# Performance work log

Hardware: AMD Instinct MI355X
Metric: run time of the kernel (lower is better)

## Reference

```python
import jax, jax.numpy as jnp
import numpy as np
import math

B, N, CS, CZ, CH, H, PQK, PV = 1, 1024, 384, 128, 16, 12, 4, 8
INF, EPS = 1e5, 1e-8


def quat_to_rot(q):
    w, x, y, z = q[..., 0], q[..., 1], q[..., 2], q[..., 3]
    r = jnp.stack([
        1 - 2 * (y * y + z * z), 2 * (x * y - w * z), 2 * (x * z + w * y),
        2 * (x * y + w * z), 1 - 2 * (x * x + z * z), 2 * (y * z - w * x),
        2 * (x * z - w * y), 2 * (y * z + w * x), 1 - 2 * (x * x + y * y),
    ], axis=-1)
    return r.reshape(q.shape[:-1] + (3, 3))


def setup_inputs() -> dict:
    key = jax.random.key(0)
    ks = jax.random.split(key, 12)
    sc = 0.02
    s = jax.random.normal(ks[0], (B, N, CS), jnp.float32)
    z = jax.random.normal(ks[1], (B, N, N, CZ), jnp.float32)
    quat = jax.random.normal(ks[2], (B, N, 4), jnp.float32)
    rot = quat_to_rot(quat / jnp.linalg.norm(quat, axis=-1, keepdims=True))
    trans = jax.random.normal(ks[3], (B, N, 3), jnp.float32)
    mask = jnp.ones((B, N), jnp.float32)
    wq = jax.random.normal(ks[4], (CS, H * CH), jnp.float32) * sc
    bq = jnp.zeros((H * CH,), jnp.float32)
    wkv = jax.random.normal(ks[5], (CS, 2 * H * CH), jnp.float32) * sc
    bkv = jnp.zeros((2 * H * CH,), jnp.float32)
    wqp = jax.random.normal(ks[6], (CS, H * PQK * 3), jnp.float32) * sc
    bqp = jnp.zeros((H * PQK * 3,), jnp.float32)
    wkvp = jax.random.normal(ks[7], (CS, H * (PQK + PV) * 3), jnp.float32) * sc
    bkvp = jnp.zeros((H * (PQK + PV) * 3,), jnp.float32)
    wb = jax.random.normal(ks[8], (CZ, H), jnp.float32) * sc
    bb = jnp.zeros((H,), jnp.float32)
    head_w = jax.random.normal(ks[9], (H,), jnp.float32) * 0.1 + 0.5413  # softplus^-1(1)
    dcat = H * (CZ + CH + PV * 4)
    wout = jax.random.normal(ks[10], (dcat, CS), jnp.float32) * sc
    bout = jnp.zeros((CS,), jnp.float32)
    return dict(s=s, z=z, rot=rot, trans=trans, mask=mask, wq=wq, bq=bq,
                wkv=wkv, bkv=bkv, wqp=wqp, bqp=bqp, wkvp=wkvp, bkvp=bkvp,
                wb=wb, bb=bb, head_w=head_w, wout=wout, bout=bout)


def reference(s, z, rot, trans, mask, wq, bq, wkv, bkv, wqp, bqp, wkvp, bkvp,
              wb, bb, head_w, wout, bout):
    # scalar q/k/v: [B,N,H,CH]
    q = (s @ wq + bq).reshape(B, N, H, CH)
    kv = (s @ wkv + bkv).reshape(B, N, H, 2 * CH)
    k, v = kv[..., :CH], kv[..., CH:]

    def make_pts(raw, P):
        # raw layout: [x-coords | y-coords | z-coords], each of width H*P
        pts = jnp.swapaxes(raw.reshape(B, N, 3, H * P), -1, -2)  # [B,N,H*P,3]
        pts = jnp.einsum('bnxy,bnpy->bnpx', rot, pts) + trans[:, :, None, :]
        return pts.reshape(B, N, H, P, 3)

    q_pts = make_pts(s @ wqp + bqp, PQK)                 # [B,N,H,PQK,3] global frame
    kv_pts = make_pts(s @ wkvp + bkvp, PQK + PV)
    k_pts, v_pts = kv_pts[..., :PQK, :], kv_pts[..., PQK:, :]

    # scalar attention + pair bias: [B,H,N,N]
    a = jnp.einsum('bihc,bjhc->bhij', q, k) * math.sqrt(1.0 / (3 * CH))
    bias = z @ wb + bb                                    # [B,N,N,H]
    a = a + math.sqrt(1.0 / 3) * jnp.transpose(bias, (0, 3, 1, 2))

    # point attention via ||q-k||^2 = |q|^2 + |k|^2 - 2 q.k (summed over pts & xyz)
    hw = jax.nn.softplus(head_w) * math.sqrt(1.0 / (3 * (PQK * 9.0 / 2)))  # [H]
    qn = jnp.sum(q_pts ** 2, axis=(-1, -2))               # [B,N,H]
    kn = jnp.sum(k_pts ** 2, axis=(-1, -2))
    cross = jnp.einsum('bihpx,bjhpx->bhij', q_pts, k_pts)
    sqd = (jnp.transpose(qn, (0, 2, 1))[..., None]
           + jnp.transpose(kn, (0, 2, 1))[:, :, None, :]
           - 2.0 * cross)                                 # [B,H,N,N]
    a = a - 0.5 * hw[None, :, None, None] * sqd

    sqm = INF * (mask[:, :, None] * mask[:, None, :] - 1.0)  # [B,N,N]
    a = jax.nn.softmax(a + sqm[:, None], axis=-1)

    # outputs
    o = jnp.einsum('bhij,bjhc->bihc', a, v).reshape(B, N, H * CH)
    o_pt = jnp.einsum('bhij,bjhpx->bihpx', a, v_pts)      # [B,N,H,PV,3] global
    o_pt = jnp.einsum('bnyx,bnhpy->bnhpx', rot, o_pt - trans[:, :, None, None, :])  # invert_apply
    o_pt_norm = jnp.sqrt(jnp.sum(o_pt ** 2, axis=-1) + EPS).reshape(B, N, H * PV)
    o_pt3 = o_pt.reshape(B, N, H * PV, 3)
    o_pair = jnp.einsum('bhij,bijc->bihc', a, z).reshape(B, N, H * CZ)

    cat = jnp.concatenate(
        [o, o_pt3[..., 0], o_pt3[..., 1], o_pt3[..., 2], o_pt_norm, o_pair], axis=-1)
    return cat @ wout + bout
```

## Files before the change

### kernel.cpp

```cpp
#include <hip/hip_runtime.h>
#include <hip/hip_bf16.h>
#include <math.h>

#define NN   1024
#define CS   384
#define CZ   128
#define HH   12
#define HCH  192
#define QPR  144
#define DCAT 2112
#define PROJW 1152
#define INF_ 100000.0f

#define SC_QK 0.14433756729740643f
#define SC_B  0.5773502691896258f
#define SC_PT 0.13608276348795434f

__device__ __forceinline__ float dot4(float4 a, float4 b) {
  return a.x * b.x + a.y * b.y + a.z * b.z + a.w * b.w;
}
__device__ __forceinline__ float bf2f(unsigned short u) {
  unsigned int v = ((unsigned int)u) << 16;
  float f; __builtin_memcpy(&f, &v, 4); return f;
}
__device__ __forceinline__ unsigned short f2bf(float f) {
  __hip_bfloat16 h = __float2bfloat16(f);
  unsigned short u; __builtin_memcpy(&u, &h, 2); return u;
}

__global__ void prep(const float* __restrict__ wb, const float* __restrict__ head_w,
                     float* __restrict__ wb_t, float* __restrict__ hw)
{
  int t = threadIdx.x;
  for (int idx = t; idx < CZ * HH; idx += 256) {
    int c = idx % HH == idx % HH ? idx / HH : 0;
    int h = idx - c * HH;
    wb_t[h * CZ + c] = wb[idx];
  }
  if (t < HH) {
    float x = head_w[t];
    float sp = (x > 20.f) ? x : log1pf(__expf(x));
    hw[t] = sp * SC_PT;
  }
}

__global__ __launch_bounds__(256) void proj_all(
    const float* __restrict__ s,
    const float* __restrict__ wq, const float* __restrict__ bq,
    const float* __restrict__ wkv, const float* __restrict__ bkv,
    const float* __restrict__ wqp, const float* __restrict__ bqp,
    const float* __restrict__ wkvp, const float* __restrict__ bkvp,
    float* __restrict__ proj)
{
  __shared__ float s_lds[8 * CS];
  const int n0 = blockIdx.x * 8;
  for (int idx = threadIdx.x; idx < 8 * CS; idx += 256)
    s_lds[idx] = s[(size_t)(n0 + idx / CS) * CS + (idx % CS)];
  __syncthreads();

  const int gc = blockIdx.y * 128 + (threadIdx.x & 31) * 4;
  const int rg = threadIdx.x >> 5;
  const float* wp; const float* bp; int OUT, lc;
  if (gc < 192)      { wp = wq;   bp = bq;   OUT = 192; lc = gc; }
  else if (gc < 576) { wp = wkv;  bp = bkv;  OUT = 384; lc = gc - 192; }
  else if (gc < 720) { wp = wqp;  bp = bqp;  OUT = 144; lc = gc - 576; }
  else               { wp = wkvp; bp = bkvp; OUT = 432; lc = gc - 720; }

  float a0 = 0.f, a1 = 0.f, a2 = 0.f, a3 = 0.f;
  const float* srow = &s_lds[rg * CS];
#pragma unroll 4
  for (int kk = 0; kk < CS; kk++) {
    float sv = srow[kk];
    float4 w4 = *reinterpret_cast<const float4*>(&wp[(size_t)kk * OUT + lc]);
    a0 += sv * w4.x; a1 += sv * w4.y; a2 += sv * w4.z; a3 += sv * w4.w;
  }
  float* o = proj + (size_t)(n0 + rg) * PROJW + gc;
  o[0] = a0 + bp[lc]; o[1] = a1 + bp[lc + 1];
  o[2] = a2 + bp[lc + 2]; o[3] = a3 + bp[lc + 3];
}

__global__ __launch_bounds__(256) void ipa_transform(
    const float* __restrict__ proj, const float* __restrict__ rot,
    const float* __restrict__ trans,
    float* __restrict__ kc, float* __restrict__ vc,
    float* __restrict__ q_pts, float* __restrict__ kpc,
    float* __restrict__ vpc, float* __restrict__ qn, float* __restrict__ knc)
{
  const int n = blockIdx.x, tid = threadIdx.x;
  const float* pr = proj + (size_t)n * PROJW;
  __shared__ float R[9], T[3], sq_q[48], sq_k[48];
  if (tid < 9) R[tid] = rot[n * 9 + tid];
  if (tid < 3) T[tid] = trans[n * 3 + tid];
  __syncthreads();
  if (tid < HCH) {
    int h = tid >> 4, c = tid & 15;
    kc[(size_t)(h * 16 + c) * NN + n] = pr[192 + h * 32 + c];
    vc[(size_t)(h * 16 + c) * NN + n] = pr[192 + h * 32 + 16 + c];
  }
  if (tid < 48) {
    float r0 = pr[576 + tid], r1 = pr[576 + 48 + tid], r2 = pr[576 + 96 + tid];
    float x = R[0] * r0 + R[1] * r1 + R[2] * r2 + T[0];
    float y = R[3] * r0 + R[4] * r1 + R[5] * r2 + T[1];
    float z = R[6] * r0 + R[7] * r1 + R[8] * r2 + T[2];
    q_pts[(size_t)n * QPR + tid * 3 + 0] = x;
    q_pts[(size_t)n * QPR + tid * 3 + 1] = y;
    q_pts[(size_t)n * QPR + tid * 3 + 2] = z;
    sq_q[tid] = x * x + y * y + z * z;
  }
  if (tid >= 64 && tid < 208) {
    int t = tid - 64;
    float r0 = pr[720 + t], r1 = pr[720 + 144 + t], r2 = pr[720 + 288 + t];
    float x = R[0] * r0 + R[1] * r1 + R[2] * r2 + T[0];
    float y = R[3] * r0 + R[4] * r1 + R[5] * r2 + T[1];
    float z = R[6] * r0 + R[7] * r1 + R[8] * r2 + T[2];
    int h = t / 12, pp = t % 12;
    if (pp < 4) {
      int d = pp * 3;
      kpc[(size_t)(h * 12 + d + 0) * NN + n] = x;
      kpc[(size_t)(h * 12 + d + 1) * NN + n] = y;
      kpc[(size_t)(h * 12 + d + 2) * NN + n] = z;
      sq_k[h * 4 + pp] = x * x + y * y + z * z;
    } else {
      int d = (pp - 4) * 3;
      vpc[(size_t)(h * 24 + d + 0) * NN + n] = x;
      vpc[(size_t)(h * 24 + d + 1) * NN + n] = y;
      vpc[(size_t)(h * 24 + d + 2) * NN + n] = z;
    }
  }
  __syncthreads();
  if (tid < HH) {
    float a = 0.f, b = 0.f;
#pragma unroll
    for (int p = 0; p < 4; p++) { a += sq_q[tid * 4 + p]; b += sq_k[tid * 4 + p]; }
    qn[n * HH + tid] = a;
    knc[(size_t)tid * NN + n] = b;
  }
}

__global__ __launch_bounds__(256) void bias_pass(
    const float* __restrict__ z, const float* __restrict__ wb_t,
    __hip_bfloat16* __restrict__ B)
{
  __shared__ float wb_s[HH * CZ];
  __shared__ float bias_s[HH * 128];
  const int i = blockIdx.y;
  const int jb = blockIdx.x * 128;
  const int tid = threadIdx.x;
  const int jl = tid >> 2, csub = tid & 3;

  for (int e = tid; e < HH * CZ; e += 256) wb_s[e] = wb_t[e];
  __syncthreads();

  const float* zb = z + ((size_t)i * NN + jb + jl) * CZ + csub * 4;
  float4 zq0[8], zq1[8];
#pragma unroll
  for (int k8 = 0; k8 < 8; k8++)
    zq0[k8] = *reinterpret_cast<const float4*>(&zb[k8 * 16]);
#pragma unroll
  for (int k8 = 0; k8 < 8; k8++)
    zq1[k8] = *reinterpret_cast<const float4*>(&zb[(size_t)64 * CZ + k8 * 16]);

  float bd0[HH], bd1[HH];
#pragma unroll
  for (int h = 0; h < HH; h++) { bd0[h] = 0.f; bd1[h] = 0.f; }

#pragma unroll
  for (int k8 = 0; k8 < 8; k8++) {
    const int c = csub * 4 + k8 * 16;
#pragma unroll
    for (int h = 0; h < HH; h++) {
      float4 wv = *reinterpret_cast<const float4*>(&wb_s[h * CZ + c]);
      bd0[h] += dot4(zq0[k8], wv);
      bd1[h] += dot4(zq1[k8], wv);
    }
  }
#pragma unroll
  for (int h = 0; h < HH; h++) {
    bd0[h] += __shfl_xor(bd0[h], 1); bd0[h] += __shfl_xor(bd0[h], 2);
    bd1[h] += __shfl_xor(bd1[h], 1); bd1[h] += __shfl_xor(bd1[h], 2);
  }
  if (csub == 0) {
#pragma unroll
    for (int h = 0; h < HH; h++) {
      bias_s[h * 128 + jl] = bd0[h];
      bias_s[h * 128 + 64 + jl] = bd1[h];
    }
  }
  __syncthreads();
  for (int e = tid; e < HH * 128; e += 256) {
    int h = e >> 7, j2 = e & 127;
    B[((size_t)i * HH + h) * NN + jb + j2] = __float2bfloat16(bias_s[e]);
  }
}

__global__ __launch_bounds__(256) void ipa_attn(
    const float* __restrict__ kc, const float* __restrict__ kpc,
    const float* __restrict__ knc, const float* __restrict__ vc,
    const float* __restrict__ vpc, const float* __restrict__ proj,
    const float* __restrict__ q_pts, const float* __restrict__ qn,
    const float* __restrict__ bb, const float* __restrict__ hw,
    const float* __restrict__ mask,
    __hip_bfloat16* __restrict__ A, float* __restrict__ cat,
    float* __restrict__ optb)
{
  const int h = blockIdx.y;
  const int i = blockIdx.x * 4 + (threadIdx.x >> 6);
  const int lane = threadIdx.x & 63;

  const float* qb = proj + (size_t)i * PROJW + h * 16;
  const float4 q0 = *reinterpret_cast<const float4*>(qb);
  const float4 q1 = *reinterpret_cast<const float4*>(qb + 4);
  const float4 q2 = *reinterpret_cast<const float4*>(qb + 8);
  const float4 q3 = *reinterpret_cast<const float4*>(qb + 12);
  const float* pb = q_pts + (size_t)i * QPR + h * 12;
  const float4 p0 = *reinterpret_cast<const float4*>(pb);
  const float4 p1 = *reinterpret_cast<const float4*>(pb + 4);
  const float4 p2 = *reinterpret_cast<const float4*>(pb + 8);
  const float qnv = qn[i * HH + h];
  const float bbv = bb[h];
  const float hwv = hw[h];
  const float mi = mask[i];

  const float* kch  = kc  + (size_t)h * 16 * NN;
  const float* kpch = kpc + (size_t)h * 12 * NN;
  const float* knch = knc + (size_t)h * NN;
  const float* vch  = vc  + (size_t)h * 16 * NN;
  const float* vpch = vpc + (size_t)h * 24 * NN;
  __hip_bfloat16* Arow = A + ((size_t)i * HH + h) * NN;

  float4 av[4];
#pragma unroll
  for (int t = 0; t < 4; t++) {
    const int j = t * 256 + lane * 4;
    float4 d = {0, 0, 0, 0};
#pragma unroll
    for (int c = 0; c < 16; c++) {
      const float qc = (c < 4 ? (&q0.x)[c] : c < 8 ? (&q1.x)[c - 4]
                       : c < 12 ? (&q2.x)[c - 8] : (&q3.x)[c - 12]);
      float4 kv = *reinterpret_cast<const float4*>(&kch[(size_t)c * NN + j]);
      d.x += qc * kv.x; d.y += qc * kv.y; d.z += qc * kv.z; d.w += qc * kv.w;
    }
    float4 cr = {0, 0, 0, 0};
#pragma unroll
    for (int dd = 0; dd < 12; dd++) {
      const float pc = (dd < 4 ? (&p0.x)[dd] : dd < 8 ? (&p1.x)[dd - 4]
                        : (&p2.x)[dd - 8]);
      float4 kv = *reinterpret_cast<const float4*>(&kpch[(size_t)dd * NN + j]);
      cr.x += pc * kv.x; cr.y += pc * kv.y; cr.z += pc * kv.z; cr.w += pc * kv.w;
    }
    float4 kn4 = *reinterpret_cast<const float4*>(&knch[j]);
    ushort4 bu = *reinterpret_cast<const ushort4*>(&Arow[j]);
    float4 m4 = *reinterpret_cast<const float4*>(&mask[j]);
    av[t].x = SC_QK * d.x + SC_B * (bf2f(bu.x) + bbv)
              - 0.5f * hwv * (qnv + kn4.x - 2.f * cr.x) + INF_ * (mi * m4.x - 1.f);
    av[t].y = SC_QK * d.y + SC_B * (bf2f(bu.y) + bbv)
              - 0.5f * hwv * (qnv + kn4.y - 2.f * cr.y) + INF_ * (mi * m4.y - 1.f);
    av[t].z = SC_QK * d.z + SC_B * (bf2f(bu.z) + bbv)
              - 0.5f * hwv * (qnv + kn4.z - 2.f * cr.z) + INF_ * (mi * m4.z - 1.f);
    av[t].w = SC_QK * d.w + SC_B * (bf2f(bu.w) + bbv)
              - 0.5f * hwv * (qnv + kn4.w - 2.f * cr.w) + INF_ * (mi * m4.w - 1.f);
  }

  float m = av[0].x;
#pragma unroll
  for (int t = 0; t < 4; t++) {
    m = fmaxf(m, av[t].x); m = fmaxf(m, av[t].y);
    m = fmaxf(m, av[t].z); m = fmaxf(m, av[t].w);
  }
  for (int off = 32; off; off >>= 1) m = fmaxf(m, __shfl_xor(m, off));
  float ssum = 0.f;
#pragma unroll
  for (int t = 0; t < 4; t++) {
    av[t].x = __expf(av[t].x - m); ssum += av[t].x;
    av[t].y = __expf(av[t].y - m); ssum += av[t].y;
    av[t].z = __expf(av[t].z - m); ssum += av[t].z;
    av[t].w = __expf(av[t].w - m); ssum += av[t].w;
  }
  for (int off = 32; off; off >>= 1) ssum += __shfl_xor(ssum, off);
  const float inv = 1.f / ssum;
#pragma unroll
  for (int t = 0; t < 4; t++) {
    const int j = t * 256 + lane * 4;
    av[t].x *= inv; av[t].y *= inv; av[t].z *= inv; av[t].w *= inv;
    ushort4 st;
    st.x = f2bf(av[t].x); st.y = f2bf(av[t].y);
    st.z = f2bf(av[t].z); st.w = f2bf(av[t].w);
    *reinterpret_cast<ushort4*>(&Arow[j]) = st;
  }

  float oacc[16], wacc[24];
#pragma unroll
  for (int c = 0; c < 16; c++) oacc[c] = 0.f;
#pragma unroll
  for (int d = 0; d < 24; d++) wacc[d] = 0.f;
#pragma unroll
  for (int t = 0; t < 4; t++) {
    const int j = t * 256 + lane * 4;
    const float4 a4 = av[t];
#pragma unroll
    for (int c = 0; c < 16; c++) {
      float4 vv = *reinterpret_cast<const float4*>(&vch[(size_t)c * NN + j]);
      oacc[c] += dot4(a4, vv);
    }
#pragma unroll
    for (int d = 0; d < 24; d++) {
      float4 wv = *reinterpret_cast<const float4*>(&vpch[(size_t)d * NN + j]);
      wacc[d] += dot4(a4, wv);
    }
  }
  for (int off = 32; off; off >>= 1) {
#pragma unroll
    for (int c = 0; c < 16; c++) oacc[c] += __shfl_xor(oacc[c], off);
#pragma unroll
    for (int d = 0; d < 24; d++) wacc[d] += __shfl_xor(wacc[d], off);
  }
  if (lane == 0) {
    float* cr = cat + (size_t)i * DCAT + h * 16;
#pragma unroll
    for (int c = 0; c < 16; c++) cr[c] = oacc[c];
    float* ob = optb + ((size_t)i * HH + h) * 24;
#pragma unroll
    for (int d = 0; d < 24; d++) ob[d] = wacc[d];
  }
}

__global__ __launch_bounds__(256) void opair_pass(
    const float* __restrict__ z, const __hip_bfloat16* __restrict__ A,
    float* __restrict__ partial)
{
  __shared__ float A_ls[256 * HH];
  __shared__ float red[HH * CZ];
  const int sp = blockIdx.x, i = blockIdx.y;
  const int jb = sp * 256;
  const int tid = threadIdx.x;
  const int c4 = (tid & 31) * 4, jsub = tid >> 5;

  for (int e = tid; e < HH * 64; e += 256) {
    int h = e >> 6, j4 = (e & 63) * 4;
    ushort4 au = *reinterpret_cast<const ushort4*>(
        &A[((size_t)i * HH + h) * NN + jb + j4]);
    A_ls[(j4 + 0) * HH + h] = bf2f(au.x);
    A_ls[(j4 + 1) * HH + h] = bf2f(au.y);
    A_ls[(j4 + 2) * HH + h] = bf2f(au.z);
    A_ls[(j4 + 3) * HH + h] = bf2f(au.w);
  }
  for (int e = tid; e < HH * CZ; e += 256) red[e] = 0.f;
  __syncthreads();

  float4 acc[HH];
#pragma unroll
  for (int h = 0; h < HH; h++) acc[h] = make_float4(0.f, 0.f, 0.f, 0.f);

  const float* zrow = z + ((size_t)i * NN + jb + jsub * 32) * CZ + c4;
  const float* arow = &A_ls[jsub * 32 * HH];
  for (int j0 = 0; j0 < 32; j0 += 4) {
#pragma unroll
    for (int jj = 0; jj < 4; jj++) {
      const int j = j0 + jj;
      float4 zq = *reinterpret_cast<const float4*>(&zrow[(size_t)j * CZ]);
      float4 a0 = *reinterpret_cast<const float4*>(&arow[j * HH]);
      float4 a1 = *reinterpret_cast<const float4*>(&arow[j * HH + 4]);
      float4 a2 = *reinterpret_cast<const float4*>(&arow[j * HH + 8]);
      acc[0].x += a0.x * zq.x; acc[0].y += a0.x * zq.y;
      acc[0].z += a0.x * zq.z; acc[0].w += a0.x * zq.w;
      acc[1].x += a0.y * zq.x; acc[1].y += a0.y * zq.y;
      acc[1].z += a0.y * zq.z; acc[1].w += a0.y * zq.w;
      acc[2].x += a0.z * zq.x; acc[2].y += a0.z * zq.y;
      acc[2].z += a0.z * zq.z; acc[2].w += a0.z * zq.w;
      acc[3].x += a0.w * zq.x; acc[3].y += a0.w * zq.y;
      acc[3].z += a0.w * zq.z; acc[3].w += a0.w * zq.w;
      acc[4].x += a1.x * zq.x; acc[4].y += a1.x * zq.y;
      acc[4].z += a1.x * zq.z; acc[4].w += a1.x * zq.w;
      acc[5].x += a1.y * zq.x; acc[5].y += a1.y * zq.y;
      acc[5].z += a1.y * zq.z; acc[5].w += a1.y * zq.w;
      acc[6].x += a1.z * zq.x; acc[6].y += a1.z * zq.y;
      acc[6].z += a1.z * zq.z; acc[6].w += a1.z * zq.w;
      acc[7].x += a1.w * zq.x; acc[7].y += a1.w * zq.y;
      acc[7].z += a1.w * zq.z; acc[7].w += a1.w * zq.w;
      acc[8].x += a2.x * zq.x; acc[8].y += a2.x * zq.y;
      acc[8].z += a2.x * zq.z; acc[8].w += a2.x * zq.w;
      acc[9].x += a2.y * zq.x; acc[9].y += a2.y * zq.y;
      acc[9].z += a2.y * zq.z; acc[9].w += a2.y * zq.w;
      acc[10].x += a2.z * zq.x; acc[10].y += a2.z * zq.y;
      acc[10].z += a2.z * zq.z; acc[10].w += a2.z * zq.w;
      acc[11].x += a2.w * zq.x; acc[11].y += a2.w * zq.y;
      acc[11].z += a2.w * zq.z; acc[11].w += a2.w * zq.w;
    }
  }
  for (int s = 0; s < 8; s++) {
    __syncthreads();
    if (jsub == s) {
#pragma unroll
      for (int h = 0; h < HH; h++) {
        red[h * CZ + c4 + 0] += acc[h].x;
        red[h * CZ + c4 + 1] += acc[h].y;
        red[h * CZ + c4 + 2] += acc[h].z;
        red[h * CZ + c4 + 3] += acc[h].w;
      }
    }
  }
  __syncthreads();
  float* pp = partial + ((size_t)(i * 4 + sp)) * (HH * CZ);
  for (int e = tid; e < HH * CZ; e += 256) pp[e] = red[e];
}

__global__ __launch_bounds__(256) void opair_reduce(
    const float* __restrict__ partial, const float* __restrict__ optb,
    const float* __restrict__ rot, const float* __restrict__ trans,
    float* __restrict__ cat)
{
  const int i = blockIdx.x, tid = threadIdx.x;
  __shared__ float R_s[9], T_s[3];
  if (tid < 9) R_s[tid] = rot[i * 9 + tid];
  if (tid < 3) T_s[tid] = trans[i * 3 + tid];
  __syncthreads();

  const float* pp = partial + ((size_t)i * 4) * (HH * CZ);
  for (int e = tid; e < HH * CZ; e += 256) {
    float v = pp[e] + pp[HH * CZ + e] + pp[2 * HH * CZ + e] + pp[3 * HH * CZ + e];
    cat[(size_t)i * DCAT + 576 + e] = v;
  }
  if (tid < 96) {
    int h = tid >> 3, p = tid & 7;
    const float* ob = optb + ((size_t)i * HH + h) * 24 + p * 3;
    float gx = ob[0] - T_s[0];
    float gy = ob[1] - T_s[1];
    float gz = ob[2] - T_s[2];
    float lx = R_s[0] * gx + R_s[3] * gy + R_s[6] * gz;
    float ly = R_s[1] * gx + R_s[4] * gy + R_s[7] * gz;
    float lz = R_s[2] * gx + R_s[5] * gy + R_s[8] * gz;
    float* catr = cat + (size_t)i * DCAT;
    catr[192 + 0 * 96 + h * 8 + p] = lx;
    catr[192 + 1 * 96 + h * 8 + p] = ly;
    catr[192 + 2 * 96 + h * 8 + p] = lz;
    catr[480 + h * 8 + p] = sqrtf(lx * lx + ly * ly + lz * lz + 1e-8f);
  }
}

__global__ __launch_bounds__(256) void out_gemm(
    const float* __restrict__ cat, const float* __restrict__ wout,
    const float* __restrict__ bout, float* __restrict__ out)
{
  __shared__ float c_lds[4 * DCAT];
  const int n0 = blockIdx.x * 4;
  const int cq = blockIdx.y * 128 + (threadIdx.x & 63) * 2;
  const int rg = threadIdx.x >> 6;
  for (int idx = threadIdx.x; idx < 4 * DCAT; idx += 256) {
    int r = idx / DCAT, kk = idx - r * DCAT;
    c_lds[idx] = cat[(size_t)(n0 + r) * DCAT + kk];
  }
  __syncthreads();
  float a0 = 0.f, a1 = 0.f;
  const float* crow = &c_lds[rg * DCAT];
#pragma unroll 4
  for (int kk = 0; kk < DCAT; kk++) {
    float cv = crow[kk];
    float2 w2 = *reinterpret_cast<const float2*>(&wout[(size_t)kk * CS + cq]);
    a0 += cv * w2.x; a1 += cv * w2.y;
  }
  float* o = out + (size_t)(n0 + rg) * CS + cq;
  o[0] = a0 + bout[cq]; o[1] = a1 + bout[cq + 1];
}

extern "C" void kernel_launch(void* const* d_in, const int* in_sizes, int n_in,
                              void* d_out, int out_size, void* d_ws, size_t ws_size,
                              hipStream_t stream) {
  const float* s      = (const float*)d_in[0];
  const float* z      = (const float*)d_in[1];
  const float* rot    = (const float*)d_in[2];
  const float* trans  = (const float*)d_in[3];
  const float* mask   = (const float*)d_in[4];
  const float* wq     = (const float*)d_in[5];
  const float* bq     = (const float*)d_in[6];
  const float* wkv    = (const float*)d_in[7];
  const float* bkv    = (const float*)d_in[8];
  const float* wqp    = (const float*)d_in[9];
  const float* bqp    = (const float*)d_in[10];
  const float* wkvp   = (const float*)d_in[11];
  const float* bkvp   = (const float*)d_in[12];
  const float* wb     = (const float*)d_in[13];
  const float* bb     = (const float*)d_in[14];
  const float* head_w = (const float*)d_in[15];
  const float* wout   = (const float*)d_in[16];
  const float* bout   = (const float*)d_in[17];
  float* out = (float*)d_out;

  float* ws = (float*)d_ws;
  float* proj_buf = ws;
  float* kc_buf   = proj_buf + (size_t)NN * PROJW;
  float* vc_buf   = kc_buf + (size_t)HH * 16 * NN;
  float* kpc_buf  = vc_buf + (size_t)HH * 16 * NN;
  float* vpc_buf  = kpc_buf + (size_t)HH * 12 * NN;
  float* knc_buf  = vpc_buf + (size_t)HH * 24 * NN;
  float* qpts_buf = knc_buf + (size_t)HH * NN;
  float* qn_buf   = qpts_buf + (size_t)NN * QPR;
  float* wbt_buf  = qn_buf + NN * HH;
  float* hw_buf   = wbt_buf + HH * CZ;
  float* optb_buf = hw_buf + 16;
  float* cat_buf  = optb_buf + (size_t)NN * HH * 24;
  float* part_buf = cat_buf + (size_t)NN * DCAT;
  __hip_bfloat16* A_buf =
      (__hip_bfloat16*)(part_buf + (size_t)4 * NN * HH * CZ);

  prep<<<dim3(1), dim3(256), 0, stream>>>(wb, head_w, wbt_buf, hw_buf);
  proj_all<<<dim3(NN / 8, 9), dim3(256), 0, stream>>>(
      s, wq, bq, wkv, bkv, wqp, bqp, wkvp, bkvp, proj_buf);
  ipa_transform<<<dim3(NN), dim3(256), 0, stream>>>(
      proj_buf, rot, trans, kc_buf, vc_buf, qpts_buf, kpc_buf, vpc_buf,
      qn_buf, knc_buf);
  bias_pass<<<dim3(8, NN), dim3(256), 0, stream>>>(z, wbt_buf, A_buf);
  ipa_attn<<<dim3(NN / 4, HH), dim3(256), 0, stream>>>(
      kc_buf, kpc_buf, knc_buf, vc_buf, vpc_buf, proj_buf, qpts_buf,
      qn_buf, bb, hw_buf, mask, A_buf, cat_buf, optb_buf);
  opair_pass<<<dim3(4, NN), dim3(256), 0, stream>>>(z, A_buf, part_buf);
  opair_reduce<<<dim3(NN), dim3(256), 0, stream>>>(
      part_buf, optb_buf, rot, trans, cat_buf);
  out_gemm<<<dim3(NN / 4, 3), dim3(256), 0, stream>>>(
      cat_buf, wout, bout, out);
}
```

Before: 731.0 us.

## Register-tile projection and output GEMMs; add barriers in attention loops

The input-projection GEMM now computes 16 rows by 8 columns per block instead of 8 by 4, so each weight tile is reused across twice as many rows. The output GEMM now handles 16 rows per block and chunks K through shared memory in 352-wide slices, with 8 accumulators per thread. Both changes cut the number of times the weight matrices are re-read from L2/HBM. Barriers are also added at the start of each j-tile iteration in the attention kernel, likely to keep the waves of a block in step so they share cached K/V rows. The cost is extra synchronisation and fewer blocks in each GEMM grid.

```diff
diff --git a/kernel.cpp b/kernel.cpp
--- a/kernel.cpp
+++ b/kernel.cpp
@@ -33,7 +33,7 @@
 {
   int t = threadIdx.x;
   for (int idx = t; idx < CZ * HH; idx += 256) {
-    int c = idx % HH == idx % HH ? idx / HH : 0;
+    int c = idx / HH;
     int h = idx - c * HH;
     wb_t[h * CZ + c] = wb[idx];
   }
@@ -52,31 +52,35 @@
     const float* __restrict__ wkvp, const float* __restrict__ bkvp,
     float* __restrict__ proj)
 {
-  __shared__ float s_lds[8 * CS];
-  const int n0 = blockIdx.x * 8;
-  for (int idx = threadIdx.x; idx < 8 * CS; idx += 256)
+  __shared__ float s_lds[16 * CS];
+  const int n0 = blockIdx.x * 16;
+  for (int idx = threadIdx.x; idx < 16 * CS; idx += 256)
     s_lds[idx] = s[(size_t)(n0 + idx / CS) * CS + (idx % CS)];
   __syncthreads();
 
-  const int gc = blockIdx.y * 128 + (threadIdx.x & 31) * 4;
-  const int rg = threadIdx.x >> 5;
+  const int gc = blockIdx.y * 128 + (threadIdx.x & 15) * 8;
+  const int rg = threadIdx.x >> 4;
   const float* wp; const float* bp; int OUT, lc;
   if (gc < 192)      { wp = wq;   bp = bq;   OUT = 192; lc = gc; }
   else if (gc < 576) { wp = wkv;  bp = bkv;  OUT = 384; lc = gc - 192; }
   else if (gc < 720) { wp = wqp;  bp = bqp;  OUT = 144; lc = gc - 576; }
   else               { wp = wkvp; bp = bkvp; OUT = 432; lc = gc - 720; }
 
-  float a0 = 0.f, a1 = 0.f, a2 = 0.f, a3 = 0.f;
+  float acc[8];
+#pragma unroll
+  for (int u = 0; u < 8; u++) acc[u] = 0.f;
   const float* srow = &s_lds[rg * CS];
 #pragma unroll 4
   for (int kk = 0; kk < CS; kk++) {
     float sv = srow[kk];
-    float4 w4 = *reinterpret_cast<const float4*>(&wp[(size_t)kk * OUT + lc]);
-    a0 += sv * w4.x; a1 += sv * w4.y; a2 += sv * w4.z; a3 += sv * w4.w;
+    float4 wa = *reinterpret_cast<const float4*>(&wp[(size_t)kk * OUT + lc]);
+    float4 wb4 = *reinterpret_cast<const float4*>(&wp[(size_t)kk * OUT + lc + 4]);
+    acc[0] += sv * wa.x; acc[1] += sv * wa.y; acc[2] += sv * wa.z; acc[3] += sv * wa.w;
+    acc[4] += sv * wb4.x; acc[5] += sv * wb4.y; acc[6] += sv * wb4.z; acc[7] += sv * wb4.w;
   }
   float* o = proj + (size_t)(n0 + rg) * PROJW + gc;
-  o[0] = a0 + bp[lc]; o[1] = a1 + bp[lc + 1];
-  o[2] = a2 + bp[lc + 2]; o[3] = a3 + bp[lc + 3];
+#pragma unroll
+  for (int u = 0; u < 8; u++) o[u] = acc[u] + bp[lc + u];
 }
 
 __global__ __launch_bounds__(256) void ipa_transform(
@@ -231,6 +235,7 @@
   float4 av[4];
 #pragma unroll
   for (int t = 0; t < 4; t++) {
+    __syncthreads();
     const int j = t * 256 + lane * 4;
     float4 d = {0, 0, 0, 0};
 #pragma unroll
@@ -295,6 +300,7 @@
   for (int d = 0; d < 24; d++) wacc[d] = 0.f;
 #pragma unroll
   for (int t = 0; t < 4; t++) {
+    __syncthreads();
     const int j = t * 256 + lane * 4;
     const float4 a4 = av[t];
 #pragma unroll
@@ -437,29 +443,40 @@
   }
 }
 
+#define OKT 352
 __global__ __launch_bounds__(256) void out_gemm(
     const float* __restrict__ cat, const float* __restrict__ wout,
     const float* __restrict__ bout, float* __restrict__ out)
 {
-  __shared__ float c_lds[4 * DCAT];
-  const int n0 = blockIdx.x * 4;
-  const int cq = blockIdx.y * 128 + (threadIdx.x & 63) * 2;
-  const int rg = threadIdx.x >> 6;
-  for (int idx = threadIdx.x; idx < 4 * DCAT; idx += 256) {
-    int r = idx / DCAT, kk = idx - r * DCAT;
-    c_lds[idx] = cat[(size_t)(n0 + r) * DCAT + kk];
-  }
-  __syncthreads();
-  float a0 = 0.f, a1 = 0.f;
-  const float* crow = &c_lds[rg * DCAT];
+  __shared__ float c_lds[16 * OKT];
+  const int n0 = blockIdx.x * 16;
+  const int cq = blockIdx.y * 128 + (threadIdx.x & 15) * 8;
+  const int rg = threadIdx.x >> 4;
+  float acc[8];
+#pragma unroll
+  for (int u = 0; u < 8; u++) acc[u] = 0.f;
+
+  for (int kc = 0; kc < DCAT / OKT; kc++) {
+    __syncthreads();
+    for (int idx = threadIdx.x; idx < 16 * OKT; idx += 256) {
+      int r = idx / OKT, kk = idx - r * OKT;
+      c_lds[idx] = cat[(size_t)(n0 + r) * DCAT + kc * OKT + kk];
+    }
+    __syncthreads();
+    const float* crow = &c_lds[rg * OKT];
 #pragma unroll 4
-  for (int kk = 0; kk < DCAT; kk++) {
-    float cv = crow[kk];
-    float2 w2 = *reinterpret_cast<const float2*>(&wout[(size_t)kk * CS + cq]);
-    a0 += cv * w2.x; a1 += cv * w2.y;
+    for (int kk = 0; kk < OKT; kk++) {
+      float cv = crow[kk];
+      const float* wr = &wout[(size_t)(kc * OKT + kk) * CS + cq];
+      float4 wa = *reinterpret_cast<const float4*>(wr);
+      float4 wb4 = *reinterpret_cast<const float4*>(wr + 4);
+      acc[0] += cv * wa.x; acc[1] += cv * wa.y; acc[2] += cv * wa.z; acc[3] += cv * wa.w;
+      acc[4] += cv * wb4.x; acc[5] += cv * wb4.y; acc[6] += cv * wb4.z; acc[7] += cv * wb4.w;
+    }
   }
   float* o = out + (size_t)(n0 + rg) * CS + cq;
-  o[0] = a0 + bout[cq]; o[1] = a1 + bout[cq + 1];
+#pragma unroll
+  for (int u = 0; u < 8; u++) o[u] = acc[u] + bout[cq + u];
 }
 
 extern "C" void kernel_launch(void* const* d_in, const int* in_sizes, int n_in,
@@ -503,7 +520,7 @@
       (__hip_bfloat16*)(part_buf + (size_t)4 * NN * HH * CZ);
 
   prep<<<dim3(1), dim3(256), 0, stream>>>(wb, head_w, wbt_buf, hw_buf);
-  proj_all<<<dim3(NN / 8, 9), dim3(256), 0, stream>>>(
+  proj_all<<<dim3(NN / 16, 9), dim3(256), 0, stream>>>(
       s, wq, bq, wkv, bkv, wqp, bqp, wkvp, bkvp, proj_buf);
   ipa_transform<<<dim3(NN), dim3(256), 0, stream>>>(
       proj_buf, rot, trans, kc_buf, vc_buf, qpts_buf, kpc_buf, vpc_buf,
@@ -515,6 +532,6 @@
   opair_pass<<<dim3(4, NN), dim3(256), 0, stream>>>(z, A_buf, part_buf);
   opair_reduce<<<dim3(NN), dim3(256), 0, stream>>>(
       part_buf, optb_buf, rot, trans, cat_buf);
-  out_gemm<<<dim3(NN / 4, 3), dim3(256), 0, stream>>>(
+  out_gemm<<<dim3(NN / 16, 3), dim3(256), 0, stream>>>(
       cat_buf, wout, bout, out);
 }
```

Result: slower. 756.6 us (+3.5%).

## Split attention kernel into logits and output passes, fold prep kernel away

Applied to the files above, without the earlier changes.

Removes the tiny single-block prep kernel by doing the wb transpose inside bias_pass and computing softplus(head_w) inline in the attention kernel. Splits ipa_attn into attn_logits (computes softmax, writes bf16 A) and attn_out (re-reads A in bf16 and accumulates v and v_pts). Both get launch_bounds occupancy hints to lower register pressure. The split adds an extra launch and a reread of A, and the output accumulation now uses bf16-rounded probabilities.

```diff
diff --git a/kernel.cpp b/kernel.cpp
--- a/kernel.cpp
+++ b/kernel.cpp
@@ -26,22 +26,6 @@
 __device__ __forceinline__ unsigned short f2bf(float f) {
   __hip_bfloat16 h = __float2bfloat16(f);
   unsigned short u; __builtin_memcpy(&u, &h, 2); return u;
-}
-
-__global__ void prep(const float* __restrict__ wb, const float* __restrict__ head_w,
-                     float* __restrict__ wb_t, float* __restrict__ hw)
-{
-  int t = threadIdx.x;
-  for (int idx = t; idx < CZ * HH; idx += 256) {
-    int c = idx % HH == idx % HH ? idx / HH : 0;
-    int h = idx - c * HH;
-    wb_t[h * CZ + c] = wb[idx];
-  }
-  if (t < HH) {
-    float x = head_w[t];
-    float sp = (x > 20.f) ? x : log1pf(__expf(x));
-    hw[t] = sp * SC_PT;
-  }
 }
 
 __global__ __launch_bounds__(256) void proj_all(
@@ -138,7 +122,7 @@
 }
 
 __global__ __launch_bounds__(256) void bias_pass(
-    const float* __restrict__ z, const float* __restrict__ wb_t,
+    const float* __restrict__ z, const float* __restrict__ wb,
     __hip_bfloat16* __restrict__ B)
 {
   __shared__ float wb_s[HH * CZ];
@@ -148,7 +132,10 @@
   const int tid = threadIdx.x;
   const int jl = tid >> 2, csub = tid & 3;
 
-  for (int e = tid; e < HH * CZ; e += 256) wb_s[e] = wb_t[e];
+  for (int e = tid; e < HH * CZ; e += 256) {
+    int c = e / HH, h = e - c * HH;
+    wb_s[h * CZ + c] = wb[e];
+  }
   __syncthreads();
 
   const float* zb = z + ((size_t)i * NN + jb + jl) * CZ + csub * 4;
@@ -193,15 +180,12 @@
   }
 }
 
-__global__ __launch_bounds__(256) void ipa_attn(
+__global__ __launch_bounds__(256, 8) void attn_logits(
     const float* __restrict__ kc, const float* __restrict__ kpc,
-    const float* __restrict__ knc, const float* __restrict__ vc,
-    const float* __restrict__ vpc, const float* __restrict__ proj,
+    const float* __restrict__ knc, const float* __restrict__ proj,
     const float* __restrict__ q_pts, const float* __restrict__ qn,
-    const float* __restrict__ bb, const float* __restrict__ hw,
-    const float* __restrict__ mask,
-    __hip_bfloat16* __restrict__ A, float* __restrict__ cat,
-    float* __restrict__ optb)
+    const float* __restrict__ bb, const float* __restrict__ head_w,
+    const float* __restrict__ mask, __hip_bfloat16* __restrict__ A)
 {
   const int h = blockIdx.y;
   const int i = blockIdx.x * 4 + (threadIdx.x >> 6);
@@ -218,14 +202,13 @@
   const float4 p2 = *reinterpret_cast<const float4*>(pb + 8);
   const float qnv = qn[i * HH + h];
   const float bbv = bb[h];
-  const float hwv = hw[h];
+  const float xw = head_w[h];
+  const float hwv = ((xw > 20.f) ? xw : log1pf(__expf(xw))) * SC_PT;
   const float mi = mask[i];
 
   const float* kch  = kc  + (size_t)h * 16 * NN;
   const float* kpch = kpc + (size_t)h * 12 * NN;
   const float* knch = knc + (size_t)h * NN;
-  const float* vch  = vc  + (size_t)h * 16 * NN;
-  const float* vpch = vpc + (size_t)h * 24 * NN;
   __hip_bfloat16* Arow = A + ((size_t)i * HH + h) * NN;
 
   float4 av[4];
@@ -281,12 +264,25 @@
 #pragma unroll
   for (int t = 0; t < 4; t++) {
     const int j = t * 256 + lane * 4;
-    av[t].x *= inv; av[t].y *= inv; av[t].z *= inv; av[t].w *= inv;
     ushort4 st;
-    st.x = f2bf(av[t].x); st.y = f2bf(av[t].y);
-    st.z = f2bf(av[t].z); st.w = f2bf(av[t].w);
+    st.x = f2bf(av[t].x * inv); st.y = f2bf(av[t].y * inv);
+    st.z = f2bf(av[t].z * inv); st.w = f2bf(av[t].w * inv);
     *reinterpret_cast<ushort4*>(&Arow[j]) = st;
   }
+}
+
+__global__ __launch_bounds__(256, 8) void attn_out(
+    const float* __restrict__ vc, const float* __restrict__ vpc,
+    const __hip_bfloat16* __restrict__ A,
+    float* __restrict__ cat, float* __restrict__ optb)
+{
+  const int h = blockIdx.y;
+  const int i = blockIdx.x * 4 + (threadIdx.x >> 6);
+  const int lane = threadIdx.x & 63;
+
+  const float* vch  = vc  + (size_t)h * 16 * NN;
+  const float* vpch = vpc + (size_t)h * 24 * NN;
+  const __hip_bfloat16* Arow = A + ((size_t)i * HH + h) * NN;
 
   float oacc[16], wacc[24];
 #pragma unroll
@@ -296,7 +292,8 @@
 #pragma unroll
   for (int t = 0; t < 4; t++) {
     const int j = t * 256 + lane * 4;
-    const float4 a4 = av[t];
+    ushort4 au = *reinterpret_cast<const ushort4*>(&Arow[j]);
+    float4 a4 = make_float4(bf2f(au.x), bf2f(au.y), bf2f(au.z), bf2f(au.w));
 #pragma unroll
     for (int c = 0; c < 16; c++) {
       float4 vv = *reinterpret_cast<const float4*>(&vch[(size_t)c * NN + j]);
@@ -494,24 +491,23 @@
   float* knc_buf  = vpc_buf + (size_t)HH * 24 * NN;
   float* qpts_buf = knc_buf + (size_t)HH * NN;
   float* qn_buf   = qpts_buf + (size_t)NN * QPR;
-  float* wbt_buf  = qn_buf + NN * HH;
-  float* hw_buf   = wbt_buf + HH * CZ;
-  float* optb_buf = hw_buf + 16;
+  float* optb_buf = qn_buf + NN * HH + 16;
   float* cat_buf  = optb_buf + (size_t)NN * HH * 24;
   float* part_buf = cat_buf + (size_t)NN * DCAT;
   __hip_bfloat16* A_buf =
       (__hip_bfloat16*)(part_buf + (size_t)4 * NN * HH * CZ);
 
-  prep<<<dim3(1), dim3(256), 0, stream>>>(wb, head_w, wbt_buf, hw_buf);
   proj_all<<<dim3(NN / 8, 9), dim3(256), 0, stream>>>(
       s, wq, bq, wkv, bkv, wqp, bqp, wkvp, bkvp, proj_buf);
   ipa_transform<<<dim3(NN), dim3(256), 0, stream>>>(
       proj_buf, rot, trans, kc_buf, vc_buf, qpts_buf, kpc_buf, vpc_buf,
       qn_buf, knc_buf);
-  bias_pass<<<dim3(8, NN), dim3(256), 0, stream>>>(z, wbt_buf, A_buf);
-  ipa_attn<<<dim3(NN / 4, HH), dim3(256), 0, stream>>>(
-      kc_buf, kpc_buf, knc_buf, vc_buf, vpc_buf, proj_buf, qpts_buf,
-      qn_buf, bb, hw_buf, mask, A_buf, cat_buf, optb_buf);
+  bias_pass<<<dim3(8, NN), dim3(256), 0, stream>>>(z, wb, A_buf);
+  attn_logits<<<dim3(NN / 4, HH), dim3(256), 0, stream>>>(
+      kc_buf, kpc_buf, knc_buf, proj_buf, qpts_buf, qn_buf,
+      bb, head_w, mask, A_buf);
+  attn_out<<<dim3(NN / 4, HH), dim3(256), 0, stream>>>(
+      vc_buf, vpc_buf, A_buf, cat_buf, optb_buf);
   opair_pass<<<dim3(4, NN), dim3(256), 0, stream>>>(z, A_buf, part_buf);
   opair_reduce<<<dim3(NN), dim3(256), 0, stream>>>(
       part_buf, optb_buf, rot, trans, cat_buf);
```

New measurement: 1.092 ms. 49.4% more time.
